# Kernel tuning notes

Hardware: AMD Instinct MI355X
Metric: run time of the kernel (lower is better)

## Reference

```python
import jax, jax.numpy as jnp
import numpy as np

D_MODEL = 1024
NUM_HEADS = 16
D_K = D_MODEL // NUM_HEADS
S, B = 2048, 2


def setup_inputs() -> dict:
    key = jax.random.key(0)
    ks = jax.random.split(key, 11)
    lim = 1.0 / np.sqrt(D_MODEL)
    def lin(kw, kb):
        W = jax.random.uniform(kw, (D_MODEL, D_MODEL), jnp.float32, -lim, lim)
        b = jax.random.uniform(kb, (D_MODEL,), jnp.float32, -lim, lim)
        return W, b
    Wq, bq = lin(ks[0], ks[1])
    Wk, bk = lin(ks[2], ks[3])
    Wv, bv = lin(ks[4], ks[5])
    Wo, bo = lin(ks[6], ks[7])
    q = jax.random.normal(ks[8], (S, B, D_MODEL), jnp.float32)
    k = jax.random.normal(ks[9], (S, B, D_MODEL), jnp.float32)
    v = jax.random.normal(ks[10], (S, B, D_MODEL), jnp.float32)
    return {"q": q, "k": k, "v": v,
            "Wq": Wq, "bq": bq, "Wk": Wk, "bk": bk,
            "Wv": Wv, "bv": bv, "Wo": Wo, "bo": bo}


def reference(q, k, v, Wq, bq, Wk, bk, Wv, bv, Wo, bo):
    s, b, _ = q.shape
    scale = np.sqrt(D_K).astype(np.float32)
    # torch Linear: x @ W.T + b
    def proj(x, W, bias):
        y = jnp.einsum('sbd,ed->sbe', x, W) + bias
        # [S,B,D] -> [B,H,S,d_k]
        return y.reshape(s, b, NUM_HEADS, D_K).transpose(1, 2, 0, 3)
    Q = proj(q, Wq, bq)
    K = proj(k, Wk, bk)
    V = proj(v, Wv, bv)
    scores = jnp.einsum('bhsd,bhtd->bhst', Q, K) / scale  # [B,H,S,S]
    attn = jax.nn.softmax(scores, axis=-1)
    ctx = jnp.einsum('bhst,bhtd->bhsd', attn, V)  # [B,H,S,d_k]
    ctx = ctx.transpose(2, 0, 1, 3).reshape(s, b, NUM_HEADS * D_K)
    return jnp.einsum('sbd,ed->sbe', ctx, Wo) + bo
```

## Files before the change

kernel.cpp:

```cpp
#include <hip/hip_runtime.h>
#include <stdint.h>

typedef __attribute__((ext_vector_type(8))) short short8;
typedef __attribute__((ext_vector_type(4))) float f32x4;
typedef __attribute__((ext_vector_type(16))) float f32x16;

#define MFMA16(a, b, c) __builtin_amdgcn_mfma_f32_16x16x32_bf16((a), (b), (c), 0, 0, 0)
#define MFMA32(a, b, c) __builtin_amdgcn_mfma_f32_32x32x16_bf16((a), (b), (c), 0, 0, 0)

__device__ inline unsigned short f2bf(float x) {
  unsigned u = __float_as_uint(x);
  u = (u + 0x7FFFu + ((u >> 16) & 1u)) >> 16;
  return (unsigned short)u;
}

__device__ inline void gload16(const unsigned short* g, unsigned short* l) {
  __builtin_amdgcn_global_load_lds(
      (const __attribute__((address_space(1))) unsigned int*)g,
      (__attribute__((address_space(3))) unsigned int*)l, 16, 0, 0);
}

__device__ inline short8 lds8(const unsigned short* base, int byteoff) {
  return *reinterpret_cast<const short8*>(reinterpret_cast<const char*>(base) + byteoff);
}

__device__ inline unsigned cvtpk(float lo, float hi) {
  unsigned r;
  asm("v_cvt_pk_bf16_f32 %0, %1, %2" : "=v"(r) : "v"(lo), "v"(hi));
  return r;
}
__device__ inline void plswap(unsigned& a, unsigned& b) {
  asm volatile("v_permlane32_swap_b32 %0, %1" : "+v"(a), "+v"(b));
}
__device__ inline float swapadd(float v) {
  float a = v, b;
  asm volatile("v_mov_b32 %1, %0\n\tv_permlane32_swap_b32 %0, %1" : "+v"(a), "=&v"(b));
  return a + b;
}

__device__ inline short8 mk8(unsigned a, unsigned b, unsigned c, unsigned d) {
  union { unsigned u[4]; short8 v; } x;
  x.u[0] = a; x.u[1] = b; x.u[2] = c; x.u[3] = d;
  return x.v;
}

__device__ inline int swz(int row, int chunk) {
  return row * 128 + (((chunk) ^ (row & 7)) << 4);
}

__device__ inline void exppack(const f32x16& sv, float& lsum, short8& paLo, short8& paHi) {
  float p[16];
#pragma unroll
  for (int i = 0; i < 16; ++i) p[i] = __builtin_amdgcn_exp2f(sv[i]);
  float q8[8];
#pragma unroll
  for (int i = 0; i < 8; ++i) q8[i] = p[2 * i] + p[2 * i + 1];
#pragma unroll
  for (int s2 = 4; s2 > 0; s2 >>= 1)
#pragma unroll
    for (int i = 0; i < s2; ++i) q8[i] += q8[i + s2];
  lsum += q8[0];
  unsigned w0 = cvtpk(p[0], p[1]), w1 = cvtpk(p[2], p[3]);
  unsigned w2 = cvtpk(p[4], p[5]), w3 = cvtpk(p[6], p[7]);
  plswap(w0, w2); plswap(w1, w3);
  unsigned w4 = cvtpk(p[8], p[9]), w5 = cvtpk(p[10], p[11]);
  unsigned w6 = cvtpk(p[12], p[13]), w7 = cvtpk(p[14], p[15]);
  plswap(w4, w6); plswap(w5, w7);
  paLo = mk8(w0, w1, w2, w3);
  paHi = mk8(w4, w5, w6, w7);
}

__global__ __launch_bounds__(256) void cvt_bf16x(const float* __restrict__ a0,
                                                 const float* __restrict__ a1,
                                                 const float* __restrict__ a2,
                                                 const float* __restrict__ a3,
                                                 unsigned short* __restrict__ d, int per) {
  int y = blockIdx.y;
  const float* s = (y == 0) ? a0 : (y == 1) ? a1 : (y == 2) ? a2 : a3;
  int i = (blockIdx.x * 256 + threadIdx.x) * 8;
  if (i >= per) return;
  float4 v0 = *reinterpret_cast<const float4*>(s + i);
  float4 v1 = *reinterpret_cast<const float4*>(s + i + 4);
  short8 o;
  o[0] = (short)f2bf(v0.x); o[1] = (short)f2bf(v0.y);
  o[2] = (short)f2bf(v0.z); o[3] = (short)f2bf(v0.w);
  o[4] = (short)f2bf(v1.x); o[5] = (short)f2bf(v1.y);
  o[6] = (short)f2bf(v1.z); o[7] = (short)f2bf(v1.w);
  *reinterpret_cast<short8*>(d + (size_t)y * per + i) = o;
}

template <int MODE>
__global__ __launch_bounds__(256) void gemm_bt(
    const unsigned short* __restrict__ Abase, const unsigned short* __restrict__ Wbase,
    const float* __restrict__ bias0, const float* __restrict__ bias1,
    const float* __restrict__ bias2, unsigned short* __restrict__ ObaseBf,
    float* __restrict__ ObaseF, int M, int N, int K) {
  constexpr int CHUNK = (MODE == 0) ? 192 : 64;

  const int orig = blockIdx.x;
  const int wg = (orig & 7) * CHUNK + (orig >> 3);
  int z, bx, by;
  if (MODE == 0) {
    z = wg >> 9;
    int r = wg & 511;
    by = r & 15;
    bx = r >> 4;
  } else {
    z = 0; by = wg & 15; bx = wg >> 4;
  }

  const unsigned short* A = Abase + (size_t)z * M * K;
  const unsigned short* W = Wbase + (size_t)z * N * K;
  const float* bias = (z == 0) ? bias0 : (z == 1 ? bias1 : bias2);

  __shared__ unsigned short As[2 * 128 * 64];
  __shared__ unsigned short Bs[2 * 64 * 64];

  const int t = threadIdx.x;
  const int lane = t & 63, w = t >> 6;
  const int wm = w >> 1, wn = w & 1;
  const int m0 = bx * 128, n0 = by * 64;
  const int lrow = lane & 15, lg = lane >> 4;

  f32x4 acc[4][2] = {};

  int arow[4], acol[4], brow[2], bcol[2];
#pragma unroll
  for (int p = 0; p < 4; ++p) {
    int c = (p * 4 + w) * 64 + lane;
    arow[p] = c >> 3; acol[p] = ((c & 7) ^ (arow[p] & 7)) * 8;
  }
#pragma unroll
  for (int p = 0; p < 2; ++p) {
    int c = (p * 4 + w) * 64 + lane;
    brow[p] = c >> 3; bcol[p] = ((c & 7) ^ (brow[p] & 7)) * 8;
  }

#define STAGE_G(kt, buf)                                                              \
  {                                                                                   \
    _Pragma("unroll") for (int p = 0; p < 4; ++p)                                     \
        gload16(&A[(size_t)(m0 + arow[p]) * K + (kt) + acol[p]],                      \
                &As[(buf)*8192 + ((p * 4 + w) * 64) * 8]);                            \
    _Pragma("unroll") for (int p = 0; p < 2; ++p)                                     \
        gload16(&W[(size_t)(n0 + brow[p]) * K + (kt) + bcol[p]],                      \
                &Bs[(buf)*4096 + ((p * 4 + w) * 64) * 8]);                            \
  }

#define COMPUTE(buf)                                                                  \
  {                                                                                   \
    _Pragma("unroll") for (int kc = 0; kc < 2; ++kc) {                                \
      short8 af[4], bfr[2];                                                           \
      _Pragma("unroll") for (int i = 0; i < 4; ++i)                                   \
          af[i] = lds8(As, (buf)*16384 + swz(wm * 64 + i * 16 + lrow, kc * 4 + lg));  \
      _Pragma("unroll") for (int i = 0; i < 2; ++i)                                   \
          bfr[i] = lds8(Bs, (buf)*8192 + swz(wn * 32 + i * 16 + lrow, kc * 4 + lg));  \
      _Pragma("unroll") for (int mi = 0; mi < 4; ++mi)                                \
          _Pragma("unroll") for (int ni = 0; ni < 2; ++ni)                            \
              acc[mi][ni] = MFMA16(af[mi], bfr[ni], acc[mi][ni]);                     \
    }                                                                                 \
  }

  STAGE_G(0, 0);

  int cur = 0;
  for (int kt = 0; kt < K; kt += 64) {
    int ktn = (kt + 64 < K) ? kt + 64 : 0;
    STAGE_G(ktn, cur ^ 1);
    asm volatile("s_waitcnt vmcnt(6)" ::: "memory");
    __builtin_amdgcn_sched_barrier(0);
    __builtin_amdgcn_s_barrier();
    __builtin_amdgcn_sched_barrier(0);
    COMPUTE(cur);
    __builtin_amdgcn_sched_barrier(0);
    __builtin_amdgcn_s_barrier();
    __builtin_amdgcn_sched_barrier(0);
    cur ^= 1;
  }
#undef STAGE_G
#undef COMPUTE

  const int r0 = lg * 4;
  if (MODE == 0) {
    const float scale = (z == 0) ? 0.18033688011112042f : 1.0f;
    if (z < 2) {
      unsigned short* O = ObaseBf + (size_t)z * (size_t)M * N;
#pragma unroll
      for (int mi = 0; mi < 4; ++mi)
#pragma unroll
        for (int ni = 0; ni < 2; ++ni) {
          int e = n0 + wn * 32 + ni * 16 + lrow;
          float be = bias[e];
          int h = e >> 6, d = e & 63;
#pragma unroll
          for (int r = 0; r < 4; ++r) {
            int m = m0 + wm * 64 + mi * 16 + r0 + r;
            int s = m >> 1, bb = m & 1;
            O[(((size_t)(bb * 16 + h) * 2048 + s) << 6) + d] = f2bf((acc[mi][ni][r] + be) * scale);
          }
        }
    } else {
      unsigned short* O = ObaseBf + (size_t)2 * (size_t)M * N;
#pragma unroll
      for (int mi = 0; mi < 4; ++mi)
#pragma unroll
        for (int ni = 0; ni < 2; ++ni) {
          int e = n0 + wn * 32 + ni * 16 + lrow;
          float be = bias[e];
          int h = e >> 6, d = e & 63;
#pragma unroll
          for (int r = 0; r < 4; ++r) {
            int m = m0 + wm * 64 + mi * 16 + r0 + r;
            int s = m >> 1, bb = m & 1;
            O[(((size_t)(bb * 16 + h) * 64 + d) << 11) + s] = f2bf(acc[mi][ni][r] + be);
          }
        }
    }
  } else {
    float* O = ObaseF;
#pragma unroll
    for (int mi = 0; mi < 4; ++mi)
#pragma unroll
      for (int ni = 0; ni < 2; ++ni) {
        int e = n0 + wn * 32 + ni * 16 + lrow;
        float be = bias[e];
#pragma unroll
        for (int r = 0; r < 4; ++r) {
          int m = m0 + wm * 64 + mi * 16 + r0 + r;
          O[(size_t)m * N + e] = acc[mi][ni][r] + be;
        }
      }
  }
}

__global__ __launch_bounds__(256, 2) void attn(const unsigned short* __restrict__ Q,
                                               const unsigned short* __restrict__ K,
                                               const unsigned short* __restrict__ Vt,
                                               unsigned short* __restrict__ ctx) {
  __shared__ unsigned short Ks[4 * 4096];
  __shared__ unsigned short Vs[4 * 4096];

  const int orig = blockIdx.x;
  const int wg = ((orig & 7) << 6) + (orig >> 3);
  const int bh = wg >> 4;
  const int qb = wg & 15;

  const int t = threadIdx.x, lane = t & 63, wv = t >> 6;
  const int q0 = qb * 128 + wv * 32;
  const int q = lane & 31, hi = lane >> 5;
  const int fq = (q ^ (q >> 3)) & 7;

  const unsigned short* Qb = Q + ((size_t)bh * 2048 + q0) * 64;
  const unsigned short* Kb = K + (size_t)bh * 2048 * 64;
  const unsigned short* Vb = Vt + (size_t)bh * 64 * 2048;

  short8 qf[4];
#pragma unroll
  for (int m = 0; m < 4; ++m)
    qf[m] = *reinterpret_cast<const short8*>(&Qb[q * 64 + m * 16 + hi * 8]);

  int koff[2][4], voff[2][2][2];
#pragma unroll
  for (int st = 0; st < 2; ++st) {
    int f = fq ^ (st ? 4 : 0);
#pragma unroll
    for (int m = 0; m < 4; ++m)
      koff[st][m] = (st * 32 + q) * 128 + (((m * 2 + hi) ^ f) << 4);
  }
#pragma unroll
  for (int dh = 0; dh < 2; ++dh) {
    int f = fq ^ (dh ? 4 : 0);
#pragma unroll
    for (int st = 0; st < 2; ++st)
#pragma unroll
      for (int kc = 0; kc < 2; ++kc)
        voff[dh][st][kc] = (dh * 32 + q) * 128 + (((st * 4 + kc * 2 + hi) ^ f) << 4);
  }

  int c0 = wv * 64 + lane, c1 = (4 + wv) * 64 + lane;
  int sr0 = c0 >> 3, sr1 = c1 >> 3;
  int sc0c = ((c0 & 7) ^ ((sr0 ^ (sr0 >> 3)) & 7)) * 8;
  int sc1c = ((c1 & 7) ^ ((sr1 ^ (sr1 >> 3)) & 7)) * 8;
  const unsigned short* ks0 = Kb + (size_t)sr0 * 64 + sc0c;
  const unsigned short* ks1 = Kb + (size_t)sr1 * 64 + sc1c;
  const unsigned short* vp0 = Vb + (size_t)sr0 * 2048 + sc0c;
  const unsigned short* vp1 = Vb + (size_t)sr1 * 2048 + sc1c;

#define STAGE(tt)                                                      \
  {                                                                    \
    char* kb = (char*)Ks + ((tt) & 3) * 8192;                          \
    char* vb2 = (char*)Vs + ((tt) & 3) * 8192;                         \
    gload16(ks0, (unsigned short*)(kb + wv * 1024));                   \
    gload16(ks1, (unsigned short*)(kb + (4 + wv) * 1024));             \
    gload16(vp0, (unsigned short*)(vb2 + wv * 1024));                  \
    gload16(vp1, (unsigned short*)(vb2 + (4 + wv) * 1024));            \
    ks0 += 4096; ks1 += 4096; vp0 += 64; vp1 += 64;                    \
  }

  f32x16 oa0 = {}, oa1 = {};
  float lsum = 0.f;
  const f32x16 zero16 = {};
  f32x16 sA0 = {}, sA1 = {}, sB0, sB1;

  STAGE(0); STAGE(1); STAGE(2);
  asm volatile("s_waitcnt vmcnt(8)" ::: "memory");
  __builtin_amdgcn_s_barrier();
  __builtin_amdgcn_sched_barrier(0);
#pragma unroll
  for (int m = 0; m < 4; ++m) {
    sA0 = MFMA32(lds8(Ks, koff[0][m]), qf[m], sA0);
    sA1 = MFMA32(lds8(Ks, koff[1][m]), qf[m], sA1);
  }

#define PHASE(tcur, sC0, sC1, sN0, sN1)                                         \
  {                                                                             \
    asm volatile("s_waitcnt vmcnt(4)" ::: "memory");                            \
    __builtin_amdgcn_sched_barrier(0);                                          \
    __builtin_amdgcn_s_barrier();                                               \
    __builtin_amdgcn_sched_barrier(0);                                          \
    STAGE((tcur) + 3);                                                          \
    sN0 = zero16; sN1 = zero16;                                                 \
    __builtin_amdgcn_s_setprio(1);                                              \
    {                                                                           \
      const int so = (((tcur) + 1) & 3) * 8192;                                 \
      _Pragma("unroll") for (int m = 0; m < 4; ++m) {                           \
        sN0 = MFMA32(lds8(Ks, so + koff[0][m]), qf[m], sN0);                    \
        sN1 = MFMA32(lds8(Ks, so + koff[1][m]), qf[m], sN1);                    \
      }                                                                         \
    }                                                                           \
    short8 paL0, paH0, paL1, paH1;                                              \
    exppack(sC0, lsum, paL0, paH0);                                             \
    exppack(sC1, lsum, paL1, paH1);                                             \
    {                                                                           \
      const int vo = ((tcur) & 3) * 8192;                                       \
      oa0 = MFMA32(paL0, lds8(Vs, vo + voff[0][0][0]), oa0);                    \
      oa1 = MFMA32(paL0, lds8(Vs, vo + voff[1][0][0]), oa1);                    \
      oa0 = MFMA32(paH0, lds8(Vs, vo + voff[0][0][1]), oa0);                    \
      oa1 = MFMA32(paH0, lds8(Vs, vo + voff[1][0][1]), oa1);                    \
      oa0 = MFMA32(paL1, lds8(Vs, vo + voff[0][1][0]), oa0);                    \
      oa1 = MFMA32(paL1, lds8(Vs, vo + voff[1][1][0]), oa1);                    \
      oa0 = MFMA32(paH1, lds8(Vs, vo + voff[0][1][1]), oa0);                    \
      oa1 = MFMA32(paH1, lds8(Vs, vo + voff[1][1][1]), oa1);                    \
    }                                                                           \
    __builtin_amdgcn_s_setprio(0);                                              \
  }

  for (int it = 0; it < 15; ++it) {
    int tc = 2 * it;
    PHASE(tc, sA0, sA1, sB0, sB1);
    PHASE(tc + 1, sB0, sB1, sA0, sA1);
  }
  PHASE(30, sA0, sA1, sB0, sB1);

  {
    short8 paL0, paH0, paL1, paH1;
    exppack(sB0, lsum, paL0, paH0);
    exppack(sB1, lsum, paL1, paH1);
    const int vo = 3 * 8192;
    oa0 = MFMA32(paL0, lds8(Vs, vo + voff[0][0][0]), oa0);
    oa1 = MFMA32(paL0, lds8(Vs, vo + voff[1][0][0]), oa1);
    oa0 = MFMA32(paH0, lds8(Vs, vo + voff[0][0][1]), oa0);
    oa1 = MFMA32(paH0, lds8(Vs, vo + voff[1][0][1]), oa1);
    oa0 = MFMA32(paL1, lds8(Vs, vo + voff[0][1][0]), oa0);
    oa1 = MFMA32(paL1, lds8(Vs, vo + voff[1][1][0]), oa1);
    oa0 = MFMA32(paH1, lds8(Vs, vo + voff[0][1][1]), oa0);
    oa1 = MFMA32(paH1, lds8(Vs, vo + voff[1][1][1]), oa1);
  }
#undef PHASE
#undef STAGE

  lsum = swapadd(lsum);
  float linv = 1.0f / lsum;
  const int b = bh >> 4, h = bh & 15;
#pragma unroll
  for (int r = 0; r < 16; ++r) {
    int qr = (r & 3) + 8 * (r >> 2) + 4 * hi;
    float li = __shfl(linv, qr);
    size_t base = ((size_t)(q0 + qr) * 2 + b) * 1024 + h * 64 + q;
    ctx[base] = f2bf(oa0[r] * li);
    ctx[base + 32] = f2bf(oa1[r] * li);
  }
}

extern "C" void kernel_launch(void* const* d_in, const int* in_sizes, int n_in, void* d_out,
                              int out_size, void* d_ws, size_t ws_size, hipStream_t stream) {
  const float* q  = (const float*)d_in[0];
  const float* k  = (const float*)d_in[1];
  const float* v  = (const float*)d_in[2];
  const float* Wq = (const float*)d_in[3];
  const float* bq = (const float*)d_in[4];
  const float* Wk = (const float*)d_in[5];
  const float* bk = (const float*)d_in[6];
  const float* Wv = (const float*)d_in[7];
  const float* bv = (const float*)d_in[8];
  const float* Wo = (const float*)d_in[9];
  const float* bo = (const float*)d_in[10];

  const size_t SZ_IN = 4194304;
  const size_t SZ_W  = 1048576;
  unsigned short* ws  = (unsigned short*)d_ws;
  unsigned short* xb  = ws;
  unsigned short* Wb  = xb + 3 * SZ_IN;
  unsigned short* QKV = Wb + 4 * SZ_W;
  unsigned short* ctx = QKV + 3 * SZ_IN;

  cvt_bf16x<<<dim3(SZ_IN / 2048, 3), 256, 0, stream>>>(q, k, v, v, xb, (int)SZ_IN);
  cvt_bf16x<<<dim3(SZ_W / 2048, 4), 256, 0, stream>>>(Wq, Wk, Wv, Wo, Wb, (int)SZ_W);

  gemm_bt<0><<<1536, 256, 0, stream>>>(xb, Wb, bq, bk, bv, QKV, nullptr, 4096, 1024, 1024);
  attn<<<512, 256, 0, stream>>>(QKV, QKV + SZ_IN, QKV + 2 * SZ_IN, ctx);
  gemm_bt<1><<<512, 256, 0, stream>>>(ctx, Wb + 3 * SZ_W, bo, bo, bo, nullptr,
                                      (float*)d_out, 4096, 1024, 1024);
}
```

Baseline: 125.2 us.

## Use 128x128 tiles with 32x32 MFMA for QKV projection GEMM

Splits the templated GEMM into a dedicated QKV projection kernel and an output projection kernel. The projection kernel moves from 128x64 tiles with 16x16x32 MFMA to 128x128 tiles with 32x32x16 MFMA, with each wave holding 2x2 f32x16 accumulators. This halves the grid to 768 blocks and raises arithmetic intensity per LDS read and global load. The cost is more LDS per block (64KB double-buffered), more accumulator registers, and fewer blocks to balance across CUs.

Measured after the change: 150.1 us. 19.9% more time.

```diff
diff --git a/kernel.cpp b/kernel.cpp
--- a/kernel.cpp
+++ b/kernel.cpp
@@ -89,35 +89,139 @@
   *reinterpret_cast<short8*>(d + (size_t)y * per + i) = o;
 }
 
-template <int MODE>
-__global__ __launch_bounds__(256) void gemm_bt(
+__global__ __launch_bounds__(256) void gemm_proj(
     const unsigned short* __restrict__ Abase, const unsigned short* __restrict__ Wbase,
     const float* __restrict__ bias0, const float* __restrict__ bias1,
-    const float* __restrict__ bias2, unsigned short* __restrict__ ObaseBf,
-    float* __restrict__ ObaseF, int M, int N, int K) {
-  constexpr int CHUNK = (MODE == 0) ? 192 : 64;
-
+    const float* __restrict__ bias2, unsigned short* __restrict__ Obase) {
+  const int M = 4096, N = 1024, K = 1024;
   const int orig = blockIdx.x;
-  const int wg = (orig & 7) * CHUNK + (orig >> 3);
-  int z, bx, by;
-  if (MODE == 0) {
-    z = wg >> 9;
-    int r = wg & 511;
-    by = r & 15;
-    bx = r >> 4;
-  } else {
-    z = 0; by = wg & 15; bx = wg >> 4;
-  }
+  const int wg = (orig & 7) * 96 + (orig >> 3);
+  const int z = wg >> 8;
+  const int rr_ = wg & 255;
+  const int by = rr_ & 7, bx = rr_ >> 3;
 
   const unsigned short* A = Abase + (size_t)z * M * K;
   const unsigned short* W = Wbase + (size_t)z * N * K;
   const float* bias = (z == 0) ? bias0 : (z == 1 ? bias1 : bias2);
 
   __shared__ unsigned short As[2 * 128 * 64];
+  __shared__ unsigned short Bs[2 * 128 * 64];
+
+  const int t = threadIdx.x, lane = t & 63, w = t >> 6;
+  const int wm = w >> 1, wn = w & 1;
+  const int m0 = bx * 128, n0 = by * 128;
+  const int l31 = lane & 31, hi = lane >> 5;
+
+  f32x16 acc[2][2] = {};
+
+  int srow[4], scol[4];
+#pragma unroll
+  for (int p = 0; p < 4; ++p) {
+    int c = (p * 4 + w) * 64 + lane;
+    srow[p] = c >> 3; scol[p] = ((c & 7) ^ (srow[p] & 7)) * 8;
+  }
+  int afoff[2][4], wfoff[2][4];
+#pragma unroll
+  for (int mb = 0; mb < 2; ++mb) {
+    int rowA = wm * 64 + mb * 32 + l31;
+    int rowW = wn * 64 + mb * 32 + l31;
+#pragma unroll
+    for (int kc = 0; kc < 4; ++kc) {
+      afoff[mb][kc] = rowA * 128 + (((kc * 2 + hi) ^ (rowA & 7)) << 4);
+      wfoff[mb][kc] = rowW * 128 + (((kc * 2 + hi) ^ (rowW & 7)) << 4);
+    }
+  }
+
+#define STAGE_P(kt, buf)                                                              \
+  {                                                                                   \
+    _Pragma("unroll") for (int p = 0; p < 4; ++p)                                     \
+        gload16(&A[(size_t)(m0 + srow[p]) * K + (kt) + scol[p]],                      \
+                &As[(buf)*8192 + ((p * 4 + w) * 64) * 8]);                            \
+    _Pragma("unroll") for (int p = 0; p < 4; ++p)                                     \
+        gload16(&W[(size_t)(n0 + srow[p]) * K + (kt) + scol[p]],                      \
+                &Bs[(buf)*8192 + ((p * 4 + w) * 64) * 8]);                            \
+  }
+
+#define COMPUTE_P(buf)                                                                \
+  {                                                                                   \
+    _Pragma("unroll") for (int kc = 0; kc < 4; ++kc) {                                \
+      short8 af0 = lds8(As, (buf)*16384 + afoff[0][kc]);                              \
+      short8 af1 = lds8(As, (buf)*16384 + afoff[1][kc]);                              \
+      short8 wf0 = lds8(Bs, (buf)*16384 + wfoff[0][kc]);                              \
+      short8 wf1 = lds8(Bs, (buf)*16384 + wfoff[1][kc]);                              \
+      acc[0][0] = MFMA32(af0, wf0, acc[0][0]);                                        \
+      acc[0][1] = MFMA32(af0, wf1, acc[0][1]);                                        \
+      acc[1][0] = MFMA32(af1, wf0, acc[1][0]);                                        \
+      acc[1][1] = MFMA32(af1, wf1, acc[1][1]);                                        \
+    }                                                                                 \
+  }
+
+  STAGE_P(0, 0);
+
+  int cur = 0;
+  for (int kt = 0; kt < K; kt += 64) {
+    int ktn = (kt + 64 < K) ? kt + 64 : 0;
+    STAGE_P(ktn, cur ^ 1);
+    asm volatile("s_waitcnt vmcnt(8)" ::: "memory");
+    __builtin_amdgcn_sched_barrier(0);
+    __builtin_amdgcn_s_barrier();
+    __builtin_amdgcn_sched_barrier(0);
+    COMPUTE_P(cur);
+    __builtin_amdgcn_sched_barrier(0);
+    __builtin_amdgcn_s_barrier();
+    __builtin_amdgcn_sched_barrier(0);
+    cur ^= 1;
+  }
+#undef STAGE_P
+#undef COMPUTE_P
+
+  const float scale = (z == 0) ? 0.18033688011112042f : 1.0f;
+  if (z < 2) {
+    unsigned short* O = Obase + (size_t)z * M * N;
+#pragma unroll
+    for (int eb = 0; eb < 2; ++eb) {
+      int e = n0 + wn * 64 + eb * 32 + l31;
+      float be = bias[e];
+      int h = e >> 6, d = e & 63;
+#pragma unroll
+      for (int mb = 0; mb < 2; ++mb)
+#pragma unroll
+        for (int r = 0; r < 16; ++r) {
+          int m = m0 + wm * 64 + mb * 32 + (r & 3) + 8 * (r >> 2) + 4 * hi;
+          int s = m >> 1, bb = m & 1;
+          O[(((size_t)(bb * 16 + h) * 2048 + s) << 6) + d] = f2bf((acc[mb][eb][r] + be) * scale);
+        }
+    }
+  } else {
+    unsigned short* O = Obase + (size_t)2 * M * N;
+#pragma unroll
+    for (int eb = 0; eb < 2; ++eb) {
+      int e = n0 + wn * 64 + eb * 32 + l31;
+      float be = bias[e];
+      int h = e >> 6, d = e & 63;
+#pragma unroll
+      for (int mb = 0; mb < 2; ++mb)
+#pragma unroll
+        for (int r = 0; r < 16; ++r) {
+          int m = m0 + wm * 64 + mb * 32 + (r & 3) + 8 * (r >> 2) + 4 * hi;
+          int s = m >> 1, bb = m & 1;
+          O[(((size_t)(bb * 16 + h) * 64 + d) << 11) + s] = f2bf(acc[mb][eb][r] + be);
+        }
+    }
+  }
+}
+
+__global__ __launch_bounds__(256) void gemm_out(
+    const unsigned short* __restrict__ A, const unsigned short* __restrict__ W,
+    const float* __restrict__ bias, float* __restrict__ O, int M, int N, int K) {
+  const int orig = blockIdx.x;
+  const int wg = (orig & 7) * 64 + (orig >> 3);
+  const int by = wg & 15, bx = wg >> 4;
+
+  __shared__ unsigned short As[2 * 128 * 64];
   __shared__ unsigned short Bs[2 * 64 * 64];
 
-  const int t = threadIdx.x;
-  const int lane = t & 63, w = t >> 6;
+  const int t = threadIdx.x, lane = t & 63, w = t >> 6;
   const int wm = w >> 1, wn = w & 1;
   const int m0 = bx * 128, n0 = by * 64;
   const int lrow = lane & 15, lg = lane >> 4;
@@ -161,7 +265,6 @@
   }
 
   STAGE_G(0, 0);
-
   int cur = 0;
   for (int kt = 0; kt < K; kt += 64) {
     int ktn = (kt + 64 < K) ? kt + 64 : 0;
@@ -180,56 +283,18 @@
 #undef COMPUTE
 
   const int r0 = lg * 4;
-  if (MODE == 0) {
-    const float scale = (z == 0) ? 0.18033688011112042f : 1.0f;
-    if (z < 2) {
-      unsigned short* O = ObaseBf + (size_t)z * (size_t)M * N;
-#pragma unroll
-      for (int mi = 0; mi < 4; ++mi)
-#pragma unroll
-        for (int ni = 0; ni < 2; ++ni) {
-          int e = n0 + wn * 32 + ni * 16 + lrow;
-          float be = bias[e];
-          int h = e >> 6, d = e & 63;
-#pragma unroll
-          for (int r = 0; r < 4; ++r) {
-            int m = m0 + wm * 64 + mi * 16 + r0 + r;
-            int s = m >> 1, bb = m & 1;
-            O[(((size_t)(bb * 16 + h) * 2048 + s) << 6) + d] = f2bf((acc[mi][ni][r] + be) * scale);
-          }
-        }
-    } else {
-      unsigned short* O = ObaseBf + (size_t)2 * (size_t)M * N;
-#pragma unroll
-      for (int mi = 0; mi < 4; ++mi)
-#pragma unroll
-        for (int ni = 0; ni < 2; ++ni) {
-          int e = n0 + wn * 32 + ni * 16 + lrow;
-          float be = bias[e];
-          int h = e >> 6, d = e & 63;
-#pragma unroll
-          for (int r = 0; r < 4; ++r) {
-            int m = m0 + wm * 64 + mi * 16 + r0 + r;
-            int s = m >> 1, bb = m & 1;
-            O[(((size_t)(bb * 16 + h) * 64 + d) << 11) + s] = f2bf(acc[mi][ni][r] + be);
-          }
-        }
+#pragma unroll
+  for (int mi = 0; mi < 4; ++mi)
+#pragma unroll
+    for (int ni = 0; ni < 2; ++ni) {
+      int e = n0 + wn * 32 + ni * 16 + lrow;
+      float be = bias[e];
+#pragma unroll
+      for (int r = 0; r < 4; ++r) {
+        int m = m0 + wm * 64 + mi * 16 + r0 + r;
+        O[(size_t)m * N + e] = acc[mi][ni][r] + be;
+      }
     }
-  } else {
-    float* O = ObaseF;
-#pragma unroll
-    for (int mi = 0; mi < 4; ++mi)
-#pragma unroll
-      for (int ni = 0; ni < 2; ++ni) {
-        int e = n0 + wn * 32 + ni * 16 + lrow;
-        float be = bias[e];
-#pragma unroll
-        for (int r = 0; r < 4; ++r) {
-          int m = m0 + wm * 64 + mi * 16 + r0 + r;
-          O[(size_t)m * N + e] = acc[mi][ni][r] + be;
-        }
-      }
-  }
 }
 
 __global__ __launch_bounds__(256, 2) void attn(const unsigned short* __restrict__ Q,
@@ -406,8 +471,7 @@
   cvt_bf16x<<<dim3(SZ_IN / 2048, 3), 256, 0, stream>>>(q, k, v, v, xb, (int)SZ_IN);
   cvt_bf16x<<<dim3(SZ_W / 2048, 4), 256, 0, stream>>>(Wq, Wk, Wv, Wo, Wb, (int)SZ_W);
 
-  gemm_bt<0><<<1536, 256, 0, stream>>>(xb, Wb, bq, bk, bv, QKV, nullptr, 4096, 1024, 1024);
+  gemm_proj<<<768, 256, 0, stream>>>(xb, Wb, bq, bk, bv, QKV);
   attn<<<512, 256, 0, stream>>>(QKV, QKV + SZ_IN, QKV + 2 * SZ_IN, ctx);
-  gemm_bt<1><<<512, 256, 0, stream>>>(ctx, Wb + 3 * SZ_W, bo, bo, bo, nullptr,
-                                      (float*)d_out, 4096, 1024, 1024);
-}
+  gemm_out<<<512, 256, 0, stream>>>(ctx, Wb + 3 * SZ_W, bo, (float*)d_out, 4096, 1024, 1024);
+}
```
